# Optimization experiments

Hardware: AMD Instinct MI355X
Metric: run time of the kernel (lower is better)

The kernel has to match this reference:

```python
import jax, jax.numpy as jnp
import numpy as np

B, N, K, D, G = 4, 2048, 32, 64, 32
RADIUS = 0.8


def _linear_params(key, fin, fout):
    kw, kb = jax.random.split(key)
    lim = 1.0 / np.sqrt(fin)
    W = jax.random.uniform(kw, (fin, fout), jnp.float32, -lim, lim)
    b = jax.random.uniform(kb, (fout,), jnp.float32, -lim, lim)
    return W, b


def setup_inputs() -> dict:
    key = jax.random.key(0)
    ks = jax.random.split(key, 6)
    x = jax.random.normal(ks[0], (B, N, D), jnp.float32)
    pos = jax.random.uniform(ks[1], (B, N, 3), jnp.float32)
    W_first, b_first = _linear_params(ks[2], 3 * D, G)          # layer_first
    W1, b1 = _linear_params(ks[3], D + 1 * G, G)                # layers[0]
    W2, b2 = _linear_params(ks[4], D + 2 * G, G)                # layers[1]
    W_last, b_last = _linear_params(ks[5], D + 3 * G, G)        # layer_last
    return {"x": x, "pos": pos, "W_first": W_first, "b_first": b_first,
            "W1": W1, "b1": b1, "W2": W2, "b2": b2,
            "W_last": W_last, "b_last": b_last}


def ball_query(pos, radius, k):
    # pos: (B, N, 3). CUDA ball_query semantics: for each query point take the
    # first k points (in index order) with squared distance < radius^2; pad
    # remaining slots with the first found index. Self is always within radius.
    sq = jnp.sum(pos * pos, axis=-1)                            # (B, N)
    d2 = sq[:, :, None] + sq[:, None, :] - 2.0 * jnp.einsum("bnc,bmc->bnm", pos, pos)
    within = d2 < radius * radius                               # (B, N, N)
    n = pos.shape[1]
    cand = jnp.where(within, jnp.arange(n, dtype=jnp.int32)[None, None, :], n)
    idx = jnp.sort(cand, axis=-1)[..., :k]                      # first k hits, padded with n
    first = idx[..., :1]
    return jnp.where(idx == n, first, idx)                      # (B, N, K) int32


def reference(x, pos, W_first, b_first, W1, b1, W2, b2, W_last, b_last):
    idx = ball_query(pos, RADIUS, K)                            # (B, N, K)
    knn_feat = jax.vmap(lambda xb, ib: xb[ib])(x, idx)          # (B, N, K, D)
    x_tiled = jnp.broadcast_to(x[:, :, None, :], knn_feat.shape)
    edge_feat = jnp.concatenate([x_tiled, knn_feat, knn_feat - x_tiled], axis=-1)  # (B,N,K,3D)
    y = jnp.concatenate([jax.nn.relu(edge_feat @ W_first + b_first), x_tiled], axis=-1)  # G+D
    y = jnp.concatenate([jax.nn.relu(y @ W1 + b1), y], axis=-1)                     # 2G+D
    y = jnp.concatenate([jax.nn.relu(y @ W2 + b2), y], axis=-1)                     # 3G+D
    y = jnp.concatenate([y @ W_last + b_last, y], axis=-1)                          # 4G+D
    return jnp.max(y, axis=-2)                                  # (B, N, D + 4G)
```

## Files before the change

### kernel.cpp

```cpp
#include <hip/hip_runtime.h>
#include <hip/hip_bf16.h>

#define NB 4
#define NN 2048
#define KK 32
#define DD 64
#define R2C 0.64f

typedef __attribute__((ext_vector_type(8)))  short short8;
typedef __attribute__((ext_vector_type(16))) float f32x16;

__device__ __forceinline__ unsigned short f2bf(float f) {
    __hip_bfloat16 h = __float2bfloat16(f);
    return reinterpret_cast<unsigned short&>(h);
}

__global__ __launch_bounds__(256) void prep_all_kernel(const float* __restrict__ x,
                                                       const float* __restrict__ Wf,
                                                       const float* __restrict__ W1,
                                                       const float* __restrict__ W2,
                                                       const float* __restrict__ Wl,
                                                       const float* __restrict__ bf,
                                                       const float* __restrict__ b1,
                                                       const float* __restrict__ b2,
                                                       const float* __restrict__ bl,
                                                       unsigned short* __restrict__ xbf,
                                                       float* __restrict__ wxt,
                                                       float* __restrict__ ball,
                                                       unsigned short* __restrict__ wfrag,
                                                       float* __restrict__ out) {
    int blk = blockIdx.x;
    if (blk < 512) {
        int t = blk * 256 + threadIdx.x;
        float4 v = ((const float4*)x)[t];
        ushort4 o = make_ushort4(f2bf(v.x), f2bf(v.y), f2bf(v.z), f2bf(v.w));
        *(ushort4*)(xbf + 4 * (size_t)t) = o;
        int q = t >> 4, j = (t & 15) << 2;
        *(float4*)(out + (size_t)q * 192 + 128 + j) = v;
    } else if (blk < 544) {
        int t = (blk - 512) * 256 + threadIdx.x;
        int ch = t >> 6, j = t & 63;
        int L = ch >> 5, c = ch & 31;
        float v;
        if (L == 0)      v = Wf[j * 32 + c] - Wf[(128 + j) * 32 + c];
        else if (L == 1) v = W1[(32 + j) * 32 + c];
        else if (L == 2) v = W2[(64 + j) * 32 + c];
        else             v = Wl[(96 + j) * 32 + c];
        wxt[ch * 64 + j] = v;
        if (j == 0) ball[ch] = (L == 0 ? bf[c] : L == 1 ? b1[c] : L == 2 ? b2[c] : bl[c]);
    } else {
        int t = (blk - 544) * 256 + threadIdx.x;
        int f = t >> 6, l = t & 63;
        int c = l & 31, g = l >> 5;
        unsigned short* dst = wfrag + (size_t)(f * 64 + l) * 8;
#pragma unroll
        for (int j = 0; j < 8; ++j) {
            int kl = 8 * g + j;
            float v;
            if (f < 4)       { int rr = 16 * f + kl;             v = Wf[(64 + rr) * 32 + c] + Wf[(128 + rr) * 32 + c]; }
            else if (f < 6)  { int rr = 16 * (f - 4) + kl;       v = W1[rr * 32 + c]; }
            else if (f < 8)  { int rr = 16 * (f - 6) + kl;       v = W2[rr * 32 + c]; }
            else if (f < 10) { int rr = 32 + 16 * (f - 8) + kl;  v = W2[rr * 32 + c]; }
            else if (f < 12) { int rr = 16 * (f - 10) + kl;      v = Wl[rr * 32 + c]; }
            else if (f < 14) { int rr = 32 + 16 * (f - 12) + kl; v = Wl[rr * 32 + c]; }
            else             { int rr = 64 + 16 * (f - 14) + kl; v = Wl[rr * 32 + c]; }
            dst[j] = f2bf(v);
        }
    }
}

#define HSTRIDE 40

__device__ __forceinline__ void post_layer(const f32x16& acc, float bs,
                                           unsigned short* hl, int col, int g,
                                           float& mx, short8& f0, short8& f1) {
    float v[16];
#pragma unroll
    for (int p = 0; p < 16; ++p) v[p] = fmaxf(acc[p] + bs, 0.0f);
    float m = v[0];
#pragma unroll
    for (int p = 1; p < 16; ++p) m = fmaxf(m, v[p]);
    mx = fmaxf(m, __shfl_xor(m, 32));
#pragma unroll
    for (int p = 0; p < 16; ++p) {
        int r = (p & 3) + 8 * (p >> 2) + 4 * g;
        hl[r * HSTRIDE + col] = f2bf(v[p]);
    }
    const unsigned short* row = hl + col * HSTRIDE;
    f0 = *(const short8*)(row + 8 * g);
    f1 = *(const short8*)(row + 16 + 8 * g);
}

__device__ __forceinline__ void l0_mfma(const unsigned short* __restrict__ xbf, int row,
                                        int g, int lane, const short8* wl, f32x16& acc) {
#pragma unroll
    for (int p = 0; p < 16; ++p) acc[p] = 0.0f;
    const short8* xrow = (const short8*)(xbf + (size_t)row * DD + g * 8);
    short8 k0 = xrow[0], k1 = xrow[2], k2 = xrow[4], k3 = xrow[6];
    acc = __builtin_amdgcn_mfma_f32_32x32x16_bf16(k0, wl[0 * 64 + lane], acc, 0, 0, 0);
    acc = __builtin_amdgcn_mfma_f32_32x32x16_bf16(k1, wl[1 * 64 + lane], acc, 0, 0, 0);
    acc = __builtin_amdgcn_mfma_f32_32x32x16_bf16(k2, wl[2 * 64 + lane], acc, 0, 0, 0);
    acc = __builtin_amdgcn_mfma_f32_32x32x16_bf16(k3, wl[3 * 64 + lane], acc, 0, 0, 0);
}

__device__ __forceinline__ void l1_mfma(const short8* hf, int lane, const short8* wl, f32x16& acc) {
#pragma unroll
    for (int p = 0; p < 16; ++p) acc[p] = 0.0f;
    acc = __builtin_amdgcn_mfma_f32_32x32x16_bf16(hf[0], wl[4 * 64 + lane], acc, 0, 0, 0);
    acc = __builtin_amdgcn_mfma_f32_32x32x16_bf16(hf[1], wl[5 * 64 + lane], acc, 0, 0, 0);
}

__device__ __forceinline__ void l2_mfma(const short8* h1, const short8* h0,
                                        int lane, const short8* wl, f32x16& acc) {
#pragma unroll
    for (int p = 0; p < 16; ++p) acc[p] = 0.0f;
    acc = __builtin_amdgcn_mfma_f32_32x32x16_bf16(h1[0], wl[6 * 64 + lane], acc, 0, 0, 0);
    acc = __builtin_amdgcn_mfma_f32_32x32x16_bf16(h1[1], wl[7 * 64 + lane], acc, 0, 0, 0);
    acc = __builtin_amdgcn_mfma_f32_32x32x16_bf16(h0[0], wl[8 * 64 + lane], acc, 0, 0, 0);
    acc = __builtin_amdgcn_mfma_f32_32x32x16_bf16(h0[1], wl[9 * 64 + lane], acc, 0, 0, 0);
}

__device__ __forceinline__ void l3_mfma(const short8* h2, const short8* h1, const short8* h0,
                                        int lane, const short8* wl, f32x16& acc) {
#pragma unroll
    for (int p = 0; p < 16; ++p) acc[p] = 0.0f;
    acc = __builtin_amdgcn_mfma_f32_32x32x16_bf16(h2[0], wl[10 * 64 + lane], acc, 0, 0, 0);
    acc = __builtin_amdgcn_mfma_f32_32x32x16_bf16(h2[1], wl[11 * 64 + lane], acc, 0, 0, 0);
    acc = __builtin_amdgcn_mfma_f32_32x32x16_bf16(h1[0], wl[12 * 64 + lane], acc, 0, 0, 0);
    acc = __builtin_amdgcn_mfma_f32_32x32x16_bf16(h1[1], wl[13 * 64 + lane], acc, 0, 0, 0);
    acc = __builtin_amdgcn_mfma_f32_32x32x16_bf16(h0[0], wl[14 * 64 + lane], acc, 0, 0, 0);
    acc = __builtin_amdgcn_mfma_f32_32x32x16_bf16(h0[1], wl[15 * 64 + lane], acc, 0, 0, 0);
}

__global__ __launch_bounds__(256, 2) void fused_kernel(const float* __restrict__ x,
                                                       const float* __restrict__ pos,
                                                       const unsigned short* __restrict__ xbf,
                                                       const unsigned short* __restrict__ wfrag,
                                                       const float* __restrict__ wxt,
                                                       const float* __restrict__ ball,
                                                       float* __restrict__ out) {
    __shared__ unsigned short hlds[4][4][32 * HSTRIDE];
    __shared__ int nbrs[4][4][KK];
    __shared__ unsigned short lwf[16 * 64 * 8];
    int wid = threadIdx.x >> 6, lane = threadIdx.x & 63;
    int qp = __builtin_amdgcn_readfirstlane(blockIdx.x * 4 + wid);
    int q0 = qp << 2;
    int col = lane & 31, g = lane >> 5;
    int b = q0 >> 11, n0 = q0 & (NN - 1);

    {
        const float4* src = (const float4*)wfrag;
        float4* dst = (float4*)lwf;
#pragma unroll
        for (int i = 0; i < 4; ++i) dst[threadIdx.x + 256 * i] = src[threadIdx.x + 256 * i];
    }

    const float* xq0 = x + (size_t)q0 * DD;
    float balA = ball[lane], balB = ball[64 + lane];
    float aA[4] = {balA, balA, balA, balA};
    float aB[4] = {balB, balB, balB, balB};
    const float4* wA = (const float4*)(wxt + (size_t)lane * DD);
    const float4* wB = (const float4*)(wxt + (size_t)(64 + lane) * DD);
#pragma unroll
    for (int j0 = 0; j0 < 16; ++j0) {
        float4 a4 = wA[j0], b4 = wB[j0];
#pragma unroll
        for (int t = 0; t < 4; ++t) {
            const float* xr = xq0 + t * DD + 4 * j0;
            float x0 = xr[0], x1 = xr[1], x2 = xr[2], x3 = xr[3];
            aA[t] = fmaf(x0, a4.x, aA[t]); aA[t] = fmaf(x1, a4.y, aA[t]);
            aA[t] = fmaf(x2, a4.z, aA[t]); aA[t] = fmaf(x3, a4.w, aA[t]);
            aB[t] = fmaf(x0, b4.x, aB[t]); aB[t] = fmaf(x1, b4.y, aB[t]);
            aB[t] = fmaf(x2, b4.z, aB[t]); aB[t] = fmaf(x3, b4.w, aB[t]);
        }
    }
    float bs0[4], bs1[4], bs2[4], bs3[4];
#pragma unroll
    for (int t = 0; t < 4; ++t) {
        bs0[t] = __shfl(aA[t], col, 64); bs1[t] = __shfl(aA[t], 32 + col, 64);
        bs2[t] = __shfl(aB[t], col, 64); bs3[t] = __shfl(aB[t], 32 + col, 64);
    }

    const float* pb = pos + (size_t)b * NN * 3;
    float qxv[4], qyv[4], qzv[4], sq4[4];
#pragma unroll
    for (int t = 0; t < 4; ++t) {
        int n = n0 + t;
        qxv[t] = pb[3 * n]; qyv[t] = pb[3 * n + 1]; qzv[t] = pb[3 * n + 2];
        sq4[t] = __fadd_rn(__fadd_rn(__fmul_rn(qxv[t], qxv[t]), __fmul_rn(qyv[t], qyv[t])),
                           __fmul_rn(qzv[t], qzv[t]));
    }
    int cnt[4] = {0, 0, 0, 0};
    unsigned long long ltmask = (1ULL << lane) - 1ULL;
    for (int m0 = 0; m0 < NN; m0 += 64) {
        if (cnt[0] >= KK && cnt[1] >= KK && cnt[2] >= KK && cnt[3] >= KK) break;
        int m = m0 + lane;
        float mx3 = pb[3 * m], my3 = pb[3 * m + 1], mz3 = pb[3 * m + 2];
        float sqm = __fadd_rn(__fadd_rn(__fmul_rn(mx3, mx3), __fmul_rn(my3, my3)), __fmul_rn(mz3, mz3));
#pragma unroll
        for (int t = 0; t < 4; ++t) {
            if (cnt[t] < KK) {
                float dot = __fadd_rn(__fadd_rn(__fmul_rn(qxv[t], mx3), __fmul_rn(qyv[t], my3)),
                                      __fmul_rn(qzv[t], mz3));
                float d2 = __fsub_rn(__fadd_rn(sq4[t], sqm), __fmul_rn(2.0f, dot));
                bool hit = d2 < R2C;
                unsigned long long mask = __ballot(hit);
                if (hit) {
                    int p = cnt[t] + (int)__popcll(mask & ltmask);
                    if (p < KK) nbrs[wid][t][p] = m;
                }
                cnt[t] = __builtin_amdgcn_readfirstlane(cnt[t] + (int)__popcll(mask));
            }
        }
    }
    int nbn[4];
#pragma unroll
    for (int t = 0; t < 4; ++t) nbn[t] = nbrs[wid][t][col < cnt[t] ? col : 0];

    __syncthreads();
    const short8* wl = (const short8*)lwf;
    unsigned short* hl0 = hlds[wid][0];
    unsigned short* hl1 = hlds[wid][1];
    unsigned short* hl2 = hlds[wid][2];
    unsigned short* hl3 = hlds[wid][3];

    f32x16 a0, a1, a2, a3;
    float mx0[4], mx1[4], mx2[4];
    short8 h0f[4][2], h1f[4][2], h2f[4][2];

    l0_mfma(xbf, b * NN + nbn[0], g, lane, wl, a0);
    l0_mfma(xbf, b * NN + nbn[1], g, lane, wl, a1);
    post_layer(a0, bs0[0], hl0, col, g, mx0[0], h0f[0][0], h0f[0][1]);
    l0_mfma(xbf, b * NN + nbn[2], g, lane, wl, a2);
    post_layer(a1, bs0[1], hl1, col, g, mx0[1], h0f[1][0], h0f[1][1]);
    l0_mfma(xbf, b * NN + nbn[3], g, lane, wl, a3);
    post_layer(a2, bs0[2], hl2, col, g, mx0[2], h0f[2][0], h0f[2][1]);
    post_layer(a3, bs0[3], hl3, col, g, mx0[3], h0f[3][0], h0f[3][1]);

    l1_mfma(h0f[0], lane, wl, a0);
    l1_mfma(h0f[1], lane, wl, a1);
    post_layer(a0, bs1[0], hl0, col, g, mx1[0], h1f[0][0], h1f[0][1]);
    l1_mfma(h0f[2], lane, wl, a2);
    post_layer(a1, bs1[1], hl1, col, g, mx1[1], h1f[1][0], h1f[1][1]);
    l1_mfma(h0f[3], lane, wl, a3);
    post_layer(a2, bs1[2], hl2, col, g, mx1[2], h1f[2][0], h1f[2][1]);
    post_layer(a3, bs1[3], hl3, col, g, mx1[3], h1f[3][0], h1f[3][1]);

    l2_mfma(h1f[0], h0f[0], lane, wl, a0);
    l2_mfma(h1f[1], h0f[1], lane, wl, a1);
    post_layer(a0, bs2[0], hl0, col, g, mx2[0], h2f[0][0], h2f[0][1]);
    l2_mfma(h1f[2], h0f[2], lane, wl, a2);
    post_layer(a1, bs2[1], hl1, col, g, mx2[1], h2f[1][0], h2f[1][1]);
    l2_mfma(h1f[3], h0f[3], lane, wl, a3);
    post_layer(a2, bs2[2], hl2, col, g, mx2[2], h2f[2][0], h2f[2][1]);
    post_layer(a3, bs2[3], hl3, col, g, mx2[3], h2f[3][0], h2f[3][1]);

    float m3[4];
    l3_mfma(h2f[0], h1f[0], h0f[0], lane, wl, a0);
    l3_mfma(h2f[1], h1f[1], h0f[1], lane, wl, a1);
    {
        float m = a0[0] + bs3[0];
#pragma unroll
        for (int p = 1; p < 16; ++p) m = fmaxf(m, a0[p] + bs3[0]);
        m3[0] = fmaxf(m, __shfl_xor(m, 32));
    }
    l3_mfma(h2f[2], h1f[2], h0f[2], lane, wl, a2);
    {
        float m = a1[0] + bs3[1];
#pragma unroll
        for (int p = 1; p < 16; ++p) m = fmaxf(m, a1[p] + bs3[1]);
        m3[1] = fmaxf(m, __shfl_xor(m, 32));
    }
    l3_mfma(h2f[3], h1f[3], h0f[3], lane, wl, a3);
    {
        float m = a2[0] + bs3[2];
#pragma unroll
        for (int p = 1; p < 16; ++p) m = fmaxf(m, a2[p] + bs3[2]);
        m3[2] = fmaxf(m, __shfl_xor(m, 32));
    }
    {
        float m = a3[0] + bs3[3];
#pragma unroll
        for (int p = 1; p < 16; ++p) m = fmaxf(m, a3[p] + bs3[3]);
        m3[3] = fmaxf(m, __shfl_xor(m, 32));
    }

    if (g == 0) {
#pragma unroll
        for (int t = 0; t < 4; ++t) {
            float* o = out + (size_t)(q0 + t) * 192;
            o[col]      = m3[t];
            o[32 + col] = mx2[t];
            o[64 + col] = mx1[t];
            o[96 + col] = mx0[t];
        }
    }
}

extern "C" void kernel_launch(void* const* d_in, const int* in_sizes, int n_in,
                              void* d_out, int out_size, void* d_ws, size_t ws_size,
                              hipStream_t stream) {
    const float* x   = (const float*)d_in[0];
    const float* pos = (const float*)d_in[1];
    const float* Wf  = (const float*)d_in[2];
    const float* bf  = (const float*)d_in[3];
    const float* W1  = (const float*)d_in[4];
    const float* b1  = (const float*)d_in[5];
    const float* W2  = (const float*)d_in[6];
    const float* b2  = (const float*)d_in[7];
    const float* Wl  = (const float*)d_in[8];
    const float* bl  = (const float*)d_in[9];
    float* out = (float*)d_out;

    char* ws = (char*)d_ws;
    float*          wxt   = (float*)ws;
    float*          ballp = (float*)(ws + 32768);
    unsigned short* wfrag = (unsigned short*)(ws + 40960);
    unsigned short* xbf   = (unsigned short*)(ws + (1u << 20));

    hipLaunchKernelGGL(prep_all_kernel, dim3(548), dim3(256), 0, stream,
                       x, Wf, W1, W2, Wl, bf, b1, b2, bl, xbf, wxt, ballp, wfrag, out);
    hipLaunchKernelGGL(fused_kernel, dim3(512), dim3(256), 0, stream,
                       x, pos, xbf, wfrag, wxt, ballp, out);
}
```

Before: 27.85 us.

## Fold prep kernel into fused kernel, converting weights and neighbor features in-kernel

Removes the separate prep launch. Each block now builds the bf16 MFMA weight fragments in LDS directly from the fp32 weights, and gathers neighbor rows of x in fp32, converting them to bf16 in registers. The per-query x-projection weights are read straight from the original weight layout, and the x passthrough columns of the output are written by the fused kernel. This saves a kernel launch and the intermediate workspace traffic, at the cost of redundant weight conversion in every block and twice the gather bytes for fp32 neighbor rows.

```diff
diff --git a/kernel.cpp b/kernel.cpp
--- a/kernel.cpp
+++ b/kernel.cpp
@@ -15,47 +15,93 @@
     return reinterpret_cast<unsigned short&>(h);
 }
 
-__global__ __launch_bounds__(256) void prep_all_kernel(const float* __restrict__ x,
+#define HSTRIDE 40
+
+__device__ __forceinline__ void post_layer(const f32x16& acc, float bs,
+                                           unsigned short* hl, int col, int g,
+                                           float& mx, short8& f0, short8& f1) {
+    float v[16];
+#pragma unroll
+    for (int p = 0; p < 16; ++p) v[p] = fmaxf(acc[p] + bs, 0.0f);
+    float m = v[0];
+#pragma unroll
+    for (int p = 1; p < 16; ++p) m = fmaxf(m, v[p]);
+    mx = fmaxf(m, __shfl_xor(m, 32));
+#pragma unroll
+    for (int p = 0; p < 16; ++p) {
+        int r = (p & 3) + 8 * (p >> 2) + 4 * g;
+        hl[r * HSTRIDE + col] = f2bf(v[p]);
+    }
+    const unsigned short* row = hl + col * HSTRIDE;
+    f0 = *(const short8*)(row + 8 * g);
+    f1 = *(const short8*)(row + 16 + 8 * g);
+}
+
+__device__ __forceinline__ short8 cvt8(const float* __restrict__ p) {
+    float4 a = ((const float4*)p)[0];
+    float4 b = ((const float4*)p)[1];
+    short8 r;
+    r[0] = (short)f2bf(a.x); r[1] = (short)f2bf(a.y); r[2] = (short)f2bf(a.z); r[3] = (short)f2bf(a.w);
+    r[4] = (short)f2bf(b.x); r[5] = (short)f2bf(b.y); r[6] = (short)f2bf(b.z); r[7] = (short)f2bf(b.w);
+    return r;
+}
+
+__device__ __forceinline__ void l1_mfma(const short8* hf, int lane, const short8* wl, f32x16& acc) {
+#pragma unroll
+    for (int p = 0; p < 16; ++p) acc[p] = 0.0f;
+    acc = __builtin_amdgcn_mfma_f32_32x32x16_bf16(hf[0], wl[4 * 64 + lane], acc, 0, 0, 0);
+    acc = __builtin_amdgcn_mfma_f32_32x32x16_bf16(hf[1], wl[5 * 64 + lane], acc, 0, 0, 0);
+}
+
+__device__ __forceinline__ void l2_mfma(const short8* h1, const short8* h0,
+                                        int lane, const short8* wl, f32x16& acc) {
+#pragma unroll
+    for (int p = 0; p < 16; ++p) acc[p] = 0.0f;
+    acc = __builtin_amdgcn_mfma_f32_32x32x16_bf16(h1[0], wl[6 * 64 + lane], acc, 0, 0, 0);
+    acc = __builtin_amdgcn_mfma_f32_32x32x16_bf16(h1[1], wl[7 * 64 + lane], acc, 0, 0, 0);
+    acc = __builtin_amdgcn_mfma_f32_32x32x16_bf16(h0[0], wl[8 * 64 + lane], acc, 0, 0, 0);
+    acc = __builtin_amdgcn_mfma_f32_32x32x16_bf16(h0[1], wl[9 * 64 + lane], acc, 0, 0, 0);
+}
+
+__device__ __forceinline__ void l3_mfma(const short8* h2, const short8* h1, const short8* h0,
+                                        int lane, const short8* wl, f32x16& acc) {
+#pragma unroll
+    for (int p = 0; p < 16; ++p) acc[p] = 0.0f;
+    acc = __builtin_amdgcn_mfma_f32_32x32x16_bf16(h2[0], wl[10 * 64 + lane], acc, 0, 0, 0);
+    acc = __builtin_amdgcn_mfma_f32_32x32x16_bf16(h2[1], wl[11 * 64 + lane], acc, 0, 0, 0);
+    acc = __builtin_amdgcn_mfma_f32_32x32x16_bf16(h1[0], wl[12 * 64 + lane], acc, 0, 0, 0);
+    acc = __builtin_amdgcn_mfma_f32_32x32x16_bf16(h1[1], wl[13 * 64 + lane], acc, 0, 0, 0);
+    acc = __builtin_amdgcn_mfma_f32_32x32x16_bf16(h0[0], wl[14 * 64 + lane], acc, 0, 0, 0);
+    acc = __builtin_amdgcn_mfma_f32_32x32x16_bf16(h0[1], wl[15 * 64 + lane], acc, 0, 0, 0);
+}
+
+__global__ __launch_bounds__(256, 2) void fused_kernel(const float* __restrict__ x,
+                                                       const float* __restrict__ pos,
                                                        const float* __restrict__ Wf,
+                                                       const float* __restrict__ bfv,
                                                        const float* __restrict__ W1,
+                                                       const float* __restrict__ b1,
                                                        const float* __restrict__ W2,
+                                                       const float* __restrict__ b2,
                                                        const float* __restrict__ Wl,
-                                                       const float* __restrict__ bf,
-                                                       const float* __restrict__ b1,
-                                                       const float* __restrict__ b2,
                                                        const float* __restrict__ bl,
-                                                       unsigned short* __restrict__ xbf,
-                                                       float* __restrict__ wxt,
-                                                       float* __restrict__ ball,
-                                                       unsigned short* __restrict__ wfrag,
                                                        float* __restrict__ out) {
-    int blk = blockIdx.x;
-    if (blk < 512) {
-        int t = blk * 256 + threadIdx.x;
-        float4 v = ((const float4*)x)[t];
-        ushort4 o = make_ushort4(f2bf(v.x), f2bf(v.y), f2bf(v.z), f2bf(v.w));
-        *(ushort4*)(xbf + 4 * (size_t)t) = o;
-        int q = t >> 4, j = (t & 15) << 2;
-        *(float4*)(out + (size_t)q * 192 + 128 + j) = v;
-    } else if (blk < 544) {
-        int t = (blk - 512) * 256 + threadIdx.x;
-        int ch = t >> 6, j = t & 63;
-        int L = ch >> 5, c = ch & 31;
-        float v;
-        if (L == 0)      v = Wf[j * 32 + c] - Wf[(128 + j) * 32 + c];
-        else if (L == 1) v = W1[(32 + j) * 32 + c];
-        else if (L == 2) v = W2[(64 + j) * 32 + c];
-        else             v = Wl[(96 + j) * 32 + c];
-        wxt[ch * 64 + j] = v;
-        if (j == 0) ball[ch] = (L == 0 ? bf[c] : L == 1 ? b1[c] : L == 2 ? b2[c] : bl[c]);
-    } else {
-        int t = (blk - 544) * 256 + threadIdx.x;
-        int f = t >> 6, l = t & 63;
-        int c = l & 31, g = l >> 5;
-        unsigned short* dst = wfrag + (size_t)(f * 64 + l) * 8;
+    __shared__ unsigned short hlds[4][4][32 * HSTRIDE];
+    __shared__ int nbrs[4][4][KK];
+    __shared__ unsigned short lwf[16 * 64 * 8];
+    int wid = threadIdx.x >> 6, lane = threadIdx.x & 63;
+    int qp = __builtin_amdgcn_readfirstlane(blockIdx.x * 4 + wid);
+    int q0 = qp << 2;
+    int col = lane & 31, g = lane >> 5;
+    int b = q0 >> 11, n0 = q0 & (NN - 1);
+
+    for (int e = threadIdx.x; e < 1024; e += 256) {
+        int f = e >> 6, l = e & 63;
+        int c = l & 31, g2 = l >> 5;
+        unsigned short* dst = lwf + (size_t)(f * 64 + l) * 8;
 #pragma unroll
         for (int j = 0; j < 8; ++j) {
-            int kl = 8 * g + j;
+            int kl = 8 * g2 + j;
             float v;
             if (f < 4)       { int rr = 16 * f + kl;             v = Wf[(64 + rr) * 32 + c] + Wf[(128 + rr) * 32 + c]; }
             else if (f < 6)  { int rr = 16 * (f - 4) + kl;       v = W1[rr * 32 + c]; }
@@ -67,111 +113,35 @@
             dst[j] = f2bf(v);
         }
     }
-}
-
-#define HSTRIDE 40
-
-__device__ __forceinline__ void post_layer(const f32x16& acc, float bs,
-                                           unsigned short* hl, int col, int g,
-                                           float& mx, short8& f0, short8& f1) {
-    float v[16];
-#pragma unroll
-    for (int p = 0; p < 16; ++p) v[p] = fmaxf(acc[p] + bs, 0.0f);
-    float m = v[0];
-#pragma unroll
-    for (int p = 1; p < 16; ++p) m = fmaxf(m, v[p]);
-    mx = fmaxf(m, __shfl_xor(m, 32));
-#pragma unroll
-    for (int p = 0; p < 16; ++p) {
-        int r = (p & 3) + 8 * (p >> 2) + 4 * g;
-        hl[r * HSTRIDE + col] = f2bf(v[p]);
-    }
-    const unsigned short* row = hl + col * HSTRIDE;
-    f0 = *(const short8*)(row + 8 * g);
-    f1 = *(const short8*)(row + 16 + 8 * g);
-}
-
-__device__ __forceinline__ void l0_mfma(const unsigned short* __restrict__ xbf, int row,
-                                        int g, int lane, const short8* wl, f32x16& acc) {
-#pragma unroll
-    for (int p = 0; p < 16; ++p) acc[p] = 0.0f;
-    const short8* xrow = (const short8*)(xbf + (size_t)row * DD + g * 8);
-    short8 k0 = xrow[0], k1 = xrow[2], k2 = xrow[4], k3 = xrow[6];
-    acc = __builtin_amdgcn_mfma_f32_32x32x16_bf16(k0, wl[0 * 64 + lane], acc, 0, 0, 0);
-    acc = __builtin_amdgcn_mfma_f32_32x32x16_bf16(k1, wl[1 * 64 + lane], acc, 0, 0, 0);
-    acc = __builtin_amdgcn_mfma_f32_32x32x16_bf16(k2, wl[2 * 64 + lane], acc, 0, 0, 0);
-    acc = __builtin_amdgcn_mfma_f32_32x32x16_bf16(k3, wl[3 * 64 + lane], acc, 0, 0, 0);
-}
-
-__device__ __forceinline__ void l1_mfma(const short8* hf, int lane, const short8* wl, f32x16& acc) {
-#pragma unroll
-    for (int p = 0; p < 16; ++p) acc[p] = 0.0f;
-    acc = __builtin_amdgcn_mfma_f32_32x32x16_bf16(hf[0], wl[4 * 64 + lane], acc, 0, 0, 0);
-    acc = __builtin_amdgcn_mfma_f32_32x32x16_bf16(hf[1], wl[5 * 64 + lane], acc, 0, 0, 0);
-}
-
-__device__ __forceinline__ void l2_mfma(const short8* h1, const short8* h0,
-                                        int lane, const short8* wl, f32x16& acc) {
-#pragma unroll
-    for (int p = 0; p < 16; ++p) acc[p] = 0.0f;
-    acc = __builtin_amdgcn_mfma_f32_32x32x16_bf16(h1[0], wl[6 * 64 + lane], acc, 0, 0, 0);
-    acc = __builtin_amdgcn_mfma_f32_32x32x16_bf16(h1[1], wl[7 * 64 + lane], acc, 0, 0, 0);
-    acc = __builtin_amdgcn_mfma_f32_32x32x16_bf16(h0[0], wl[8 * 64 + lane], acc, 0, 0, 0);
-    acc = __builtin_amdgcn_mfma_f32_32x32x16_bf16(h0[1], wl[9 * 64 + lane], acc, 0, 0, 0);
-}
-
-__device__ __forceinline__ void l3_mfma(const short8* h2, const short8* h1, const short8* h0,
-                                        int lane, const short8* wl, f32x16& acc) {
-#pragma unroll
-    for (int p = 0; p < 16; ++p) acc[p] = 0.0f;
-    acc = __builtin_amdgcn_mfma_f32_32x32x16_bf16(h2[0], wl[10 * 64 + lane], acc, 0, 0, 0);
-    acc = __builtin_amdgcn_mfma_f32_32x32x16_bf16(h2[1], wl[11 * 64 + lane], acc, 0, 0, 0);
-    acc = __builtin_amdgcn_mfma_f32_32x32x16_bf16(h1[0], wl[12 * 64 + lane], acc, 0, 0, 0);
-    acc = __builtin_amdgcn_mfma_f32_32x32x16_bf16(h1[1], wl[13 * 64 + lane], acc, 0, 0, 0);
-    acc = __builtin_amdgcn_mfma_f32_32x32x16_bf16(h0[0], wl[14 * 64 + lane], acc, 0, 0, 0);
-    acc = __builtin_amdgcn_mfma_f32_32x32x16_bf16(h0[1], wl[15 * 64 + lane], acc, 0, 0, 0);
-}
-
-__global__ __launch_bounds__(256, 2) void fused_kernel(const float* __restrict__ x,
-                                                       const float* __restrict__ pos,
-                                                       const unsigned short* __restrict__ xbf,
-                                                       const unsigned short* __restrict__ wfrag,
-                                                       const float* __restrict__ wxt,
-                                                       const float* __restrict__ ball,
-                                                       float* __restrict__ out) {
-    __shared__ unsigned short hlds[4][4][32 * HSTRIDE];
-    __shared__ int nbrs[4][4][KK];
-    __shared__ unsigned short lwf[16 * 64 * 8];
-    int wid = threadIdx.x >> 6, lane = threadIdx.x & 63;
-    int qp = __builtin_amdgcn_readfirstlane(blockIdx.x * 4 + wid);
-    int q0 = qp << 2;
-    int col = lane & 31, g = lane >> 5;
-    int b = q0 >> 11, n0 = q0 & (NN - 1);
-
-    {
-        const float4* src = (const float4*)wfrag;
-        float4* dst = (float4*)lwf;
-#pragma unroll
-        for (int i = 0; i < 4; ++i) dst[threadIdx.x + 256 * i] = src[threadIdx.x + 256 * i];
-    }
 
     const float* xq0 = x + (size_t)q0 * DD;
-    float balA = ball[lane], balB = ball[64 + lane];
+    bool lo = lane < 32;
+    int c0 = lane & 31;
+    const float* pA1 = lo ? (Wf + c0) : (W1 + 32 * 32 + c0);
+    const float* pA2 = lo ? (Wf + 128 * 32 + c0) : (W1 + 32 * 32 + c0);
+    float sA = lo ? -1.0f : 0.0f;
+    const float* pB1 = lo ? (W2 + 64 * 32 + c0) : (Wl + 96 * 32 + c0);
+    float balA = lo ? bfv[c0] : b1[c0];
+    float balB = lo ? b2[c0] : bl[c0];
     float aA[4] = {balA, balA, balA, balA};
     float aB[4] = {balB, balB, balB, balB};
-    const float4* wA = (const float4*)(wxt + (size_t)lane * DD);
-    const float4* wB = (const float4*)(wxt + (size_t)(64 + lane) * DD);
 #pragma unroll
     for (int j0 = 0; j0 < 16; ++j0) {
-        float4 a4 = wA[j0], b4 = wB[j0];
+        float wa[4], wb[4];
+#pragma unroll
+        for (int jj = 0; jj < 4; ++jj) {
+            int j = 4 * j0 + jj;
+            wa[jj] = fmaf(sA, pA2[j * 32], pA1[j * 32]);
+            wb[jj] = pB1[j * 32];
+        }
 #pragma unroll
         for (int t = 0; t < 4; ++t) {
             const float* xr = xq0 + t * DD + 4 * j0;
             float x0 = xr[0], x1 = xr[1], x2 = xr[2], x3 = xr[3];
-            aA[t] = fmaf(x0, a4.x, aA[t]); aA[t] = fmaf(x1, a4.y, aA[t]);
-            aA[t] = fmaf(x2, a4.z, aA[t]); aA[t] = fmaf(x3, a4.w, aA[t]);
-            aB[t] = fmaf(x0, b4.x, aB[t]); aB[t] = fmaf(x1, b4.y, aB[t]);
-            aB[t] = fmaf(x2, b4.z, aB[t]); aB[t] = fmaf(x3, b4.w, aB[t]);
+            aA[t] = fmaf(x0, wa[0], aA[t]); aA[t] = fmaf(x1, wa[1], aA[t]);
+            aA[t] = fmaf(x2, wa[2], aA[t]); aA[t] = fmaf(x3, wa[3], aA[t]);
+            aB[t] = fmaf(x0, wb[0], aB[t]); aB[t] = fmaf(x1, wb[1], aB[t]);
+            aB[t] = fmaf(x2, wb[2], aB[t]); aB[t] = fmaf(x3, wb[3], aB[t]);
         }
     }
     float bs0[4], bs1[4], bs2[4], bs3[4];
@@ -217,6 +187,14 @@
 #pragma unroll
     for (int t = 0; t < 4; ++t) nbn[t] = nbrs[wid][t][col < cnt[t] ? col : 0];
 
+    short8 xk[4][4];
+#pragma unroll
+    for (int t = 0; t < 4; ++t) {
+        const float* xrow = x + (size_t)(b * NN + nbn[t]) * DD + g * 8;
+#pragma unroll
+        for (int kf = 0; kf < 4; ++kf) xk[t][kf] = cvt8(xrow + kf * 16);
+    }
+
     __syncthreads();
     const short8* wl = (const short8*)lwf;
     unsigned short* hl0 = hlds[wid][0];
@@ -228,12 +206,18 @@
     float mx0[4], mx1[4], mx2[4];
     short8 h0f[4][2], h1f[4][2], h2f[4][2];
 
-    l0_mfma(xbf, b * NN + nbn[0], g, lane, wl, a0);
-    l0_mfma(xbf, b * NN + nbn[1], g, lane, wl, a1);
+#pragma unroll
+    for (int p = 0; p < 16; ++p) { a0[p] = 0.0f; a1[p] = 0.0f; a2[p] = 0.0f; a3[p] = 0.0f; }
+#pragma unroll
+    for (int f = 0; f < 4; ++f) a0 = __builtin_amdgcn_mfma_f32_32x32x16_bf16(xk[0][f], wl[f * 64 + lane], a0, 0, 0, 0);
+#pragma unroll
+    for (int f = 0; f < 4; ++f) a1 = __builtin_amdgcn_mfma_f32_32x32x16_bf16(xk[1][f], wl[f * 64 + lane], a1, 0, 0, 0);
     post_layer(a0, bs0[0], hl0, col, g, mx0[0], h0f[0][0], h0f[0][1]);
-    l0_mfma(xbf, b * NN + nbn[2], g, lane, wl, a2);
+#pragma unroll
+    for (int f = 0; f < 4; ++f) a2 = __builtin_amdgcn_mfma_f32_32x32x16_bf16(xk[2][f], wl[f * 64 + lane], a2, 0, 0, 0);
     post_layer(a1, bs0[1], hl1, col, g, mx0[1], h0f[1][0], h0f[1][1]);
-    l0_mfma(xbf, b * NN + nbn[3], g, lane, wl, a3);
+#pragma unroll
+    for (int f = 0; f < 4; ++f) a3 = __builtin_amdgcn_mfma_f32_32x32x16_bf16(xk[3][f], wl[f * 64 + lane], a3, 0, 0, 0);
     post_layer(a2, bs0[2], hl2, col, g, mx0[2], h0f[2][0], h0f[2][1]);
     post_layer(a3, bs0[3], hl3, col, g, mx0[3], h0f[3][0], h0f[3][1]);
 
@@ -285,15 +269,16 @@
         m3[3] = fmaxf(m, __shfl_xor(m, 32));
     }
 
-    if (g == 0) {
-#pragma unroll
-        for (int t = 0; t < 4; ++t) {
-            float* o = out + (size_t)(q0 + t) * 192;
+#pragma unroll
+    for (int t = 0; t < 4; ++t) {
+        float* o = out + (size_t)(q0 + t) * 192;
+        if (g == 0) {
             o[col]      = m3[t];
             o[32 + col] = mx2[t];
             o[64 + col] = mx1[t];
             o[96 + col] = mx0[t];
         }
+        o[128 + lane] = xq0[t * DD + lane];
     }
 }
 
@@ -312,14 +297,6 @@
     const float* bl  = (const float*)d_in[9];
     float* out = (float*)d_out;
 
-    char* ws = (char*)d_ws;
-    float*          wxt   = (float*)ws;
-    float*          ballp = (float*)(ws + 32768);
-    unsigned short* wfrag = (unsigned short*)(ws + 40960);
-    unsigned short* xbf   = (unsigned short*)(ws + (1u << 20));
-
-    hipLaunchKernelGGL(prep_all_kernel, dim3(548), dim3(256), 0, stream,
-                       x, Wf, W1, W2, Wl, bf, b1, b2, bl, xbf, wxt, ballp, wfrag, out);
     hipLaunchKernelGGL(fused_kernel, dim3(512), dim3(256), 0, stream,
-                       x, pos, xbf, wfrag, wxt, ballp, out);
-}
+                       x, pos, Wf, bf, W1, b1, W2, b2, Wl, bl, out);
+}
```

Result: faster. 26.86 us (-3.6%).
